# Performance work log

Measured on AMD Instinct MI355X. Metric: run time of the kernel, lower is better.

## Reference

```python
import jax, jax.numpy as jnp
import numpy as np

# dims: B=batch, CIN/COUT=channels, T=timesteps, K=kernel length (= T+1, since
# max_timesteps=2048 is even and CKConv bumps it to odd), DK=SIREN hidden width
B, CIN, COUT, T, DK = 32, 32, 32, 2048, 32
K = T + 1


def setup_inputs() -> dict:
    key = jax.random.key(0)
    ks = jax.random.split(key, 9)
    u = lambda k, shape, lim: jax.random.uniform(k, shape, minval=-lim, maxval=lim)
    # SIREN layer 1 (Conv1d 1->DK, k=1): first layer init uniform(-1, 1)
    w1 = u(ks[0], (DK, 1), 1.0)
    b1 = u(ks[1], (DK,), 1.0)          # torch bias init: U(-1/sqrt(fan_in)), fan_in=1
    # SIREN layer 2 (DK->DK): uniform(-sqrt(6/DK)/omega0, +), omega0=1
    siren_val = float(np.sqrt(6.0 / DK))
    w2 = u(ks[2], (DK, DK), siren_val)
    b2 = u(ks[3], (DK,), float(1.0 / np.sqrt(DK)))
    # output layer (DK -> CIN*COUT)
    w3 = u(ks[4], (CIN * COUT, DK), siren_val)
    b3 = u(ks[5], (CIN * COUT,), float(1.0 / np.sqrt(DK)))
    omega1 = jnp.asarray(1.0, jnp.float32)
    omega2 = jnp.asarray(1.0, jnp.float32)
    bias = jax.random.normal(ks[6], (COUT,), jnp.float32)   # CKConv output bias
    x = jax.random.normal(ks[7], (B, CIN, T), jnp.float32)
    rel_pos = jnp.linspace(-1.0, 1.0, K, dtype=jnp.float32)  # buffer _rel_positions
    return dict(x=x, rel_pos=rel_pos, w1=w1, b1=b1, omega1=omega1,
                w2=w2, b2=b2, omega2=omega2, w3=w3, b3=b3, bias=bias)


def reference(x, rel_pos, w1, b1, omega1, w2, b2, omega2, w3, b3, bias):
    # --- SIREN kernel network: 1x1 convs over the K positions == matmuls ---
    pos = rel_pos[None, :]                                   # (1, K)
    h = jnp.sin(omega1 * (w1 @ pos + b1[:, None]))           # (DK, K)
    h = jnp.sin(omega2 * (w2 @ h + b2[:, None]))             # (DK, K)
    kern = (w3 @ h + b3[:, None]).reshape(COUT, CIN, K)      # (COUT, CIN, K)
    # --- causal conv: left-pad by K-1 zeros, then valid cross-correlation ---
    out = jax.lax.conv_general_dilated(
        x, kern, window_strides=(1,), padding=[(K - 1, 0)],
        dimension_numbers=("NCH", "OIH", "NCH"))             # (B, COUT, T)
    return out + bias[None, :, None]
```

## Files before the change

### kernel.cpp

```cpp
#include <hip/hip_runtime.h>
#include <hip/hip_bf16.h>
#include <stdint.h>

typedef short bf16x8 __attribute__((ext_vector_type(8)));
typedef float f32x16 __attribute__((ext_vector_type(16)));

#define T 2048
#define KLEN 2049
#define DK 32
#define NCO 32
#define NCI 32
#define NB 32

#define GR 2216
#define SREF 2055
#define WT_CH 257
#define WT_ELEMS (NCI*WT_CH*NCO*8)
#define XR_ELEMS (NB*NCI*GR)

#define WT_OFF 0
#define XR_OFF (WT_ELEMS*2)
#define XRS_OFF (XR_OFF + XR_ELEMS*2)

#define CIB 528
#define GPC 1056
#define GPCP 1088
#define CPYB 17472
#define BUFB (2*CPYB)
#define LDS_TOT (2*BUFB)

__global__ __launch_bounds__(256) void gen_w(
    const float* __restrict__ rel_pos,
    const float* __restrict__ w1, const float* __restrict__ b1, const float* __restrict__ om1,
    const float* __restrict__ w2, const float* __restrict__ b2, const float* __restrict__ om2,
    const float* __restrict__ w3, const float* __restrict__ b3,
    uint16_t* __restrict__ Wt)
{
    __shared__ float h1s[8][32];
    __shared__ float h2s[8][32];
    int t = threadIdx.x;
    int dchunk = blockIdx.x;
    int dd = t >> 5, i = t & 31;
    int d = (dchunk << 3) + dd;
    float pos = (d < KLEN) ? rel_pos[2048 - d] : 0.f;
    h1s[dd][i] = sinf(om1[0] * (w1[i] * pos + b1[i]));
    __syncthreads();
    {
        float a = b2[i];
        #pragma unroll
        for (int j = 0; j < 32; ++j) a += w2[i*32 + j] * h1s[dd][j];
        h2s[dd][i] = sinf(om2[0] * a);
    }
    __syncthreads();
    for (int r = 0; r < 4; ++r) {
        int tt = t + (r << 8);
        int ci = tt >> 5, co = tt & 31;
        int coci = (co << 5) + ci;
        float w3r[32];
        #pragma unroll
        for (int j = 0; j < 8; ++j)
            *(float4*)&w3r[j*4] = *(const float4*)&w3[coci*32 + j*4];
        float bb = b3[coci];
        union { uint16_t u[8]; uint4 q; } pack;
        #pragma unroll
        for (int ddd = 0; ddd < 8; ++ddd) {
            float a = bb;
            #pragma unroll
            for (int j = 0; j < 32; ++j) a += w3r[j] * h2s[ddd][j];
            if (((dchunk << 3) + ddd) >= KLEN) a = 0.f;
            __hip_bfloat16 hv = __float2bfloat16(a);
            pack.u[ddd] = *(uint16_t*)&hv;
        }
        *(uint4*)&Wt[((ci*WT_CH + dchunk)*NCO + co) << 3] = pack.q;
    }
}

__global__ __launch_bounds__(256) void gen_x(const float* __restrict__ x,
                                             uint16_t* __restrict__ xr,
                                             uint16_t* __restrict__ xrs)
{
    int idx = blockIdx.x*256 + threadIdx.x;
    if (idx >= NB*NCI*GR) return;
    int row = idx / GR;
    int g = idx - row*GR;
    int s = SREF - g;
    float v  = (s  >= 0 && s  < T) ? x[row*T + s]  : 0.f;
    int s2 = s - 1;
    float v2 = (s2 >= 0 && s2 < T) ? x[row*T + s2] : 0.f;
    __hip_bfloat16 hv = __float2bfloat16(v);
    __hip_bfloat16 hv2 = __float2bfloat16(v2);
    xr[idx]  = *(uint16_t*)&hv;
    xrs[idx] = *(uint16_t*)&hv2;
}

__device__ __forceinline__ void gld16(const uint16_t* g, char* l)
{
    typedef const __attribute__((address_space(1))) uint32_t GU;
    typedef __attribute__((address_space(3))) uint32_t LU;
    __builtin_amdgcn_global_load_lds((GU*)g, (LU*)l, 16, 0, 0);
}

__global__ __launch_bounds__(512, 4) void conv(
    const uint16_t* __restrict__ Wt, const uint16_t* __restrict__ xr,
    const float* __restrict__ bias, float* __restrict__ out)
{
    __shared__ uint4 lds4[LDS_TOT/16];
    char* ldsb = (char*)lds4;
    float* red = (float*)lds4;
    int tid = threadIdx.x;
    int b = blockIdx.x & 31;
    int q = blockIdx.x >> 5;
    int p = q & 7;
    int th = (q < 8) ? (63 - (p << 2)) : ((p << 2) + 3);
    int nw = (th + 1) >> 2;
    int g0base = 2016 - (th << 5);
    int w = tid >> 6, lane = tid & 63, n = lane & 31, hi = lane >> 5;
    int cig = w;

    int srcE[5], dstC[5];
    #pragma unroll
    for (int k = 0; k < 5; ++k) {
        int gi = tid + (k << 9);
        if (gi < 2176) {
            int cpy = gi >= GPCP;
            int j = gi - cpy*GPCP;
            dstC[k] = cpy*CPYB + (j << 4);
            if (j < GPC) {
                int ci = (j*1986) >> 16;
                int qq = j - ci*33;
                srcE[k] = (cpy ? XR_ELEMS : 0) + (b*NCI + ci)*GR + (qq << 3);
            } else srcE[k] = 0;
        } else { srcE[k] = 0; dstC[k] = -1; }
    }

    int obase = 39 - n + (hi << 3);
    int par = obase & 1;
    int bbb = cig*CIB + par*CPYB + ((obase - par) << 1);

    f32x16 acc0, acc1, acc2, acc3;
    #pragma unroll
    for (int r = 0; r < 16; ++r) { acc0[r]=0.f; acc1[r]=0.f; acc2[r]=0.f; acc3[r]=0.f; }

    #define STAGE(BUF, GOFF) { \
        _Pragma("unroll") \
        for (int k = 0; k < 5; ++k) \
            if (dstC[k] >= 0) gld16(xr + srcE[k] + (GOFF), (BUF) + dstC[k]); }

    STAGE(ldsb, g0base)
    __syncthreads();

    for (int wi = 0; wi < nw; ++wi) {
        int cur = wi & 1;
        if (wi + 1 < nw) {
            char* bufn = ldsb + (cur ^ 1)*BUFB;
            int g0n = g0base + ((wi + 1) << 7);
            STAGE(bufn, g0n)
        }
        int dcw = wi << 4;
        const char* rbase = ldsb + cur*BUFB + bbb;

        #pragma unroll
        for (int cii = 0; cii < 4; ++cii) {
            int ci = (cii << 3) + cig;
            const uint16_t* aB = Wt + (((ci*WT_CH + dcw + hi)*NCO + n) << 3);
            bf16x8 av0 = *(const bf16x8*)(aB);
            bf16x8 av1 = *(const bf16x8*)(aB + 512);
            bf16x8 av2 = *(const bf16x8*)(aB + 1024);
            bf16x8 av3 = *(const bf16x8*)(aB + 1536);
            bf16x8 av4 = *(const bf16x8*)(aB + 2048);
            bf16x8 av5 = *(const bf16x8*)(aB + 2560);
            bf16x8 av6 = *(const bf16x8*)(aB + 3072);
            bf16x8 av7 = *(const bf16x8*)(aB + 3584);
            const char* pbase = rbase + cii*(8*CIB);

            #define RDBB(MM) union { uint32_t u_[4]; bf16x8 v; } bb; { \
                const char* pp = pbase + ((MM) << 5); \
                bb.u_[0] = *(const uint32_t*)(pp); \
                bb.u_[1] = *(const uint32_t*)(pp + 4); \
                bb.u_[2] = *(const uint32_t*)(pp + 8); \
                bb.u_[3] = *(const uint32_t*)(pp + 12); }
            #define MF(AC, AV) AC = __builtin_amdgcn_mfma_f32_32x32x16_bf16(AV, bb.v, AC, 0,0,0);

            { RDBB(0)  MF(acc0, av0) }
            { RDBB(1)  MF(acc0, av1) }
            { RDBB(2)  MF(acc0, av2) MF(acc1, av0) }
            { RDBB(3)  MF(acc0, av3) MF(acc1, av1) }
            { RDBB(4)  MF(acc0, av4) MF(acc1, av2) MF(acc2, av0) }
            { RDBB(5)  MF(acc0, av5) MF(acc1, av3) MF(acc2, av1) }
            { RDBB(6)  MF(acc0, av6) MF(acc1, av4) MF(acc2, av2) MF(acc3, av0) }
            { RDBB(7)  MF(acc0, av7) MF(acc1, av5) MF(acc2, av3) MF(acc3, av1) }
            { RDBB(8)  MF(acc1, av6) MF(acc2, av4) MF(acc3, av2) }
            { RDBB(9)  MF(acc1, av7) MF(acc2, av5) MF(acc3, av3) }
            { RDBB(10) MF(acc2, av6) MF(acc3, av4) }
            { RDBB(11) MF(acc2, av7) MF(acc3, av5) }
            { RDBB(12) MF(acc3, av6) }
            { RDBB(13) MF(acc3, av7) }
            #undef MF
            #undef RDBB
        }
        __syncthreads();
    }
    #undef STAGE

    #pragma unroll
    for (int dlt = 0; dlt < 4; ++dlt) {
        f32x16 a = (dlt == 0) ? acc0 : (dlt == 1) ? acc1 : (dlt == 2) ? acc2 : acc3;
        __syncthreads();
        if (w < 4) {
            #pragma unroll
            for (int r = 0; r < 16; ++r)
                red[(w*16 + r)*64 + lane] = a[r];
        }
        __syncthreads();
        if (w >= 4) {
            #pragma unroll
            for (int r = 0; r < 16; ++r)
                red[((w-4)*16 + r)*64 + lane] += a[r];
        }
        __syncthreads();
        int t0 = (th - dlt) << 5;
        #pragma unroll
        for (int h = 0; h < 2; ++h) {
            int e = tid + (h << 9);
            int lane_e = e & 63;
            int reg = e >> 6;
            float s = 0.f;
            #pragma unroll
            for (int ww = 0; ww < 4; ++ww) s += red[(ww*16 + reg)*64 + lane_e];
            int co = (reg & 3) + ((reg >> 2) << 3) + ((lane_e >> 5) << 2);
            int t = t0 + (lane_e & 31);
            out[(b*NCO + co)*T + t] = s + bias[co];
        }
    }
}

extern "C" void kernel_launch(void* const* d_in, const int* in_sizes, int n_in,
                              void* d_out, int out_size, void* d_ws, size_t ws_size,
                              hipStream_t stream)
{
    const float* x       = (const float*)d_in[0];
    const float* rel_pos = (const float*)d_in[1];
    const float* w1  = (const float*)d_in[2];
    const float* b1  = (const float*)d_in[3];
    const float* om1 = (const float*)d_in[4];
    const float* w2  = (const float*)d_in[5];
    const float* b2  = (const float*)d_in[6];
    const float* om2 = (const float*)d_in[7];
    const float* w3  = (const float*)d_in[8];
    const float* b3  = (const float*)d_in[9];
    const float* bias = (const float*)d_in[10];
    float* out = (float*)d_out;
    char* ws = (char*)d_ws;
    uint16_t* Wt  = (uint16_t*)(ws + WT_OFF);
    uint16_t* xrp = (uint16_t*)(ws + XR_OFF);
    uint16_t* xrs = (uint16_t*)(ws + XRS_OFF);

    hipLaunchKernelGGL(gen_w, dim3(WT_CH), dim3(256), 0, stream,
                       rel_pos, w1, b1, om1, w2, b2, om2, w3, b3, Wt);
    int n2 = NB*NCI*GR;
    hipLaunchKernelGGL(gen_x, dim3((n2+255)/256), dim3(256), 0, stream, x, xrp, xrs);
    hipLaunchKernelGGL(conv, dim3(NB*16), dim3(512), 0, stream, Wt, xrp, bias, out);
}
```

Measured before the change: 151.4 us.

## Split conv input channels across two blocks with atomic output accumulation

Each conv block now handles half of the input channels (16 instead of 32) with 256 threads, doubling the grid to 1024 blocks and halving the LDS staging footprint. Partial sums from the two halves are combined with float atomicAdd into an output buffer that a new init_out kernel pre-fills with the bias. The goal is more concurrent blocks and better load balance across CUs. The cost is an extra kernel launch, a full output write for the bias init, and atomic read-modify-write traffic. The time-tile mapping for the second half of the blocks also changes from (p<<2)+3 to (q<<2)-29, which gives the same tiles.

Measured after the change: 160.5 us. +6.0%, slower.

```diff
diff --git a/kernel.cpp b/kernel.cpp
--- a/kernel.cpp
+++ b/kernel.cpp
@@ -23,9 +23,9 @@
 #define XRS_OFF (XR_OFF + XR_ELEMS*2)
 
 #define CIB 528
-#define GPC 1056
-#define GPCP 1088
-#define CPYB 17472
+#define GPC 528
+#define GPCP 576
+#define CPYB 9280
 #define BUFB (2*CPYB)
 #define LDS_TOT (2*BUFB)
 
@@ -61,7 +61,7 @@
         for (int j = 0; j < 8; ++j)
             *(float4*)&w3r[j*4] = *(const float4*)&w3[coci*32 + j*4];
         float bb = b3[coci];
-        union { uint16_t u[8]; uint4 q; } pack;
+        union { uint16_t u[8]; uint4 qv; } pack;
         #pragma unroll
         for (int ddd = 0; ddd < 8; ++ddd) {
             float a = bb;
@@ -71,7 +71,7 @@
             __hip_bfloat16 hv = __float2bfloat16(a);
             pack.u[ddd] = *(uint16_t*)&hv;
         }
-        *(uint4*)&Wt[((ci*WT_CH + dchunk)*NCO + co) << 3] = pack.q;
+        *(uint4*)&Wt[((ci*WT_CH + dchunk)*NCO + co) << 3] = pack.qv;
     }
 }
 
@@ -93,6 +93,13 @@
     xrs[idx] = *(uint16_t*)&hv2;
 }
 
+__global__ __launch_bounds__(256) void init_out(const float* __restrict__ bias,
+                                                float* __restrict__ out)
+{
+    int i = blockIdx.x*256 + threadIdx.x;
+    out[i] = bias[(i >> 11) & 31];
+}
+
 __device__ __forceinline__ void gld16(const uint16_t* g, char* l)
 {
     typedef const __attribute__((address_space(1))) uint32_t GU;
@@ -100,18 +107,18 @@
     __builtin_amdgcn_global_load_lds((GU*)g, (LU*)l, 16, 0, 0);
 }
 
-__global__ __launch_bounds__(512, 4) void conv(
+__global__ __launch_bounds__(256, 4) void conv(
     const uint16_t* __restrict__ Wt, const uint16_t* __restrict__ xr,
-    const float* __restrict__ bias, float* __restrict__ out)
+    float* __restrict__ out)
 {
     __shared__ uint4 lds4[LDS_TOT/16];
     char* ldsb = (char*)lds4;
     float* red = (float*)lds4;
     int tid = threadIdx.x;
     int b = blockIdx.x & 31;
-    int q = blockIdx.x >> 5;
-    int p = q & 7;
-    int th = (q < 8) ? (63 - (p << 2)) : ((p << 2) + 3);
+    int q = (blockIdx.x >> 5) & 15;
+    int h = blockIdx.x >> 9;
+    int th = (q < 8) ? (63 - (q << 2)) : ((q << 2) - 29);
     int nw = (th + 1) >> 2;
     int g0base = 2016 - (th << 5);
     int w = tid >> 6, lane = tid & 63, n = lane & 31, hi = lane >> 5;
@@ -120,15 +127,15 @@
     int srcE[5], dstC[5];
     #pragma unroll
     for (int k = 0; k < 5; ++k) {
-        int gi = tid + (k << 9);
-        if (gi < 2176) {
+        int gi = tid + (k << 8);
+        if (gi < 1152) {
             int cpy = gi >= GPCP;
             int j = gi - cpy*GPCP;
             dstC[k] = cpy*CPYB + (j << 4);
             if (j < GPC) {
-                int ci = (j*1986) >> 16;
-                int qq = j - ci*33;
-                srcE[k] = (cpy ? XR_ELEMS : 0) + (b*NCI + ci)*GR + (qq << 3);
+                int cl = (j*1986) >> 16;
+                int qq = j - cl*33;
+                srcE[k] = cpy*XR_ELEMS + (b*NCI + (h << 4) + cl)*GR + (qq << 3);
             } else srcE[k] = 0;
         } else { srcE[k] = 0; dstC[k] = -1; }
     }
@@ -161,7 +168,7 @@
 
         #pragma unroll
         for (int cii = 0; cii < 4; ++cii) {
-            int ci = (cii << 3) + cig;
+            int ci = (h << 4) + (cii << 2) + cig;
             const uint16_t* aB = Wt + (((ci*WT_CH + dcw + hi)*NCO + n) << 3);
             bf16x8 av0 = *(const bf16x8*)(aB);
             bf16x8 av1 = *(const bf16x8*)(aB + 512);
@@ -171,7 +178,7 @@
             bf16x8 av5 = *(const bf16x8*)(aB + 2560);
             bf16x8 av6 = *(const bf16x8*)(aB + 3072);
             bf16x8 av7 = *(const bf16x8*)(aB + 3584);
-            const char* pbase = rbase + cii*(8*CIB);
+            const char* pbase = rbase + cii*(4*CIB);
 
             #define RDBB(MM) union { uint32_t u_[4]; bf16x8 v; } bb; { \
                 const char* pp = pbase + ((MM) << 5); \
@@ -206,30 +213,28 @@
     for (int dlt = 0; dlt < 4; ++dlt) {
         f32x16 a = (dlt == 0) ? acc0 : (dlt == 1) ? acc1 : (dlt == 2) ? acc2 : acc3;
         __syncthreads();
-        if (w < 4) {
+        if (w < 2) {
             #pragma unroll
             for (int r = 0; r < 16; ++r)
                 red[(w*16 + r)*64 + lane] = a[r];
         }
         __syncthreads();
-        if (w >= 4) {
+        if (w >= 2) {
             #pragma unroll
             for (int r = 0; r < 16; ++r)
-                red[((w-4)*16 + r)*64 + lane] += a[r];
+                red[((w-2)*16 + r)*64 + lane] += a[r];
         }
         __syncthreads();
         int t0 = (th - dlt) << 5;
         #pragma unroll
-        for (int h = 0; h < 2; ++h) {
-            int e = tid + (h << 9);
+        for (int hh = 0; hh < 4; ++hh) {
+            int e = tid + (hh << 8);
             int lane_e = e & 63;
             int reg = e >> 6;
-            float s = 0.f;
-            #pragma unroll
-            for (int ww = 0; ww < 4; ++ww) s += red[(ww*16 + reg)*64 + lane_e];
+            float s = red[(reg)*64 + lane_e] + red[(16 + reg)*64 + lane_e];
             int co = (reg & 3) + ((reg >> 2) << 3) + ((lane_e >> 5) << 2);
             int t = t0 + (lane_e & 31);
-            out[(b*NCO + co)*T + t] = s + bias[co];
+            atomicAdd(&out[(b*NCO + co)*T + t], s);
         }
     }
 }
@@ -259,5 +264,6 @@
                        rel_pos, w1, b1, om1, w2, b2, om2, w3, b3, Wt);
     int n2 = NB*NCI*GR;
     hipLaunchKernelGGL(gen_x, dim3((n2+255)/256), dim3(256), 0, stream, x, xrp, xrs);
-    hipLaunchKernelGGL(conv, dim3(NB*16), dim3(512), 0, stream, Wt, xrp, bias, out);
-}
+    hipLaunchKernelGGL(init_out, dim3(NB*NCO*T/256), dim3(256), 0, stream, bias, out);
+    hipLaunchKernelGGL(conv, dim3(NB*16*2), dim3(256), 0, stream, Wt, xrp, out);
+}
```
